# Performance work log

Hardware: AMD Instinct MI355X
Metric: run time of the kernel (lower is better)

Reference implementation:

```python
import jax, jax.numpy as jnp
import numpy as np

B, N, C = 8, 4096, 768
H, M = 12, 64          # num_heads, num_landmarks
D = C // H             # head_dim = 64


def setup_inputs() -> dict:
    key = jax.random.key(0)
    k1, k2, k3, k4 = jax.random.split(key, 4)
    s = 0.02
    return {
        "x": jax.random.normal(k1, (B, N, C), dtype=jnp.float32),
        "w_qkv": jax.random.normal(k2, (3 * C, C), dtype=jnp.float32) * s,
        "w_proj": jax.random.normal(k3, (C, C), dtype=jnp.float32) * s,
        "b_proj": jax.random.normal(k4, (C,), dtype=jnp.float32) * s,
    }


def iterative_inv(mat, n_iter=6):
    # mat: [B, H, M, M]; Newton-Schulz cubic iteration for pseudo-inverse
    I = jnp.eye(mat.shape[-1], dtype=mat.dtype)
    K = mat
    # init: K^T / max_j(sum_i K_ij)  per (B,H)
    scale = jnp.max(jnp.sum(K, axis=-2), axis=-1)[:, :, None, None]
    V = jnp.swapaxes(K, -1, -2) / scale
    for _ in range(n_iter):
        KV = K @ V
        V = 0.25 * V @ (13.0 * I - KV @ (15.0 * I - KV @ (7.0 * I - KV)))
    return V


def reference(x, w_qkv, w_proj, b_proj):
    b, n, c = x.shape
    qkv = (x @ w_qkv.T).reshape(b, n, 3, H, D).transpose(2, 0, 3, 1, 4)  # [3,B,H,N,D]
    Q, K, V = qkv[0], qkv[1], qkv[2]
    Q = Q / (D ** 0.5)
    # landmark pooling (N % M == 0 path): segment means of length N//M
    Kl = K.reshape(b, H, M, n // M, D).mean(axis=-2)  # [B,H,M,D]
    Ql = Q.reshape(b, H, M, n // M, D).mean(axis=-2)  # [B,H,M,D]
    kernel1 = jax.nn.softmax(jnp.einsum('bhnd,bhmd->bhnm', Q, Kl), axis=-1)   # [B,H,N,M]
    kernel2 = jax.nn.softmax(jnp.einsum('bhmd,bhld->bhml', Ql, Kl), axis=-1)  # [B,H,M,M]
    kernel3 = jax.nn.softmax(jnp.einsum('bhmd,bhnd->bhmn', Ql, K), axis=-1)   # [B,H,M,N]
    SV = (kernel1 @ iterative_inv(kernel2)) @ (kernel3 @ V)  # [B,H,N,D]
    SV = SV.transpose(0, 2, 1, 3).reshape(b, n, c)
    out = SV @ w_proj.T + b_proj
    out = out + V.transpose(0, 2, 1, 3).reshape(b, n, c)
    return out
```

## Files before the change

### kernel.cpp

```cpp
#include <hip/hip_runtime.h>
#include <hip/hip_bf16.h>
#include <stdint.h>

typedef __bf16 bf16;
typedef __bf16 bf16x8 __attribute__((ext_vector_type(8)));
typedef __bf16 bf16x4 __attribute__((ext_vector_type(4)));
typedef float f32x4 __attribute__((ext_vector_type(4)));

#define B_ 8
#define N_ 4096
#define C_ 768
#define H_ 12
#define M_ 64
#define D_ 64
#define NT_ 32768
#define C3_ 2304

typedef __attribute__((address_space(3))) void lds_void_t;
typedef const __attribute__((address_space(1))) void gvoid_t;

__device__ __forceinline__ void gl_lds16(const void* gsrc, void* ldst) {
  __builtin_amdgcn_global_load_lds((gvoid_t*)(uintptr_t)gsrc,
                                   (lds_void_t*)(uintptr_t)ldst, 16, 0, 0);
}

__device__ __forceinline__ f32x4 mfma16(bf16x8 a, bf16x8 b, f32x4 c) {
  return __builtin_amdgcn_mfma_f32_16x16x32_bf16(a, b, c, 0, 0, 0);
}

#define VMW8 asm volatile("s_waitcnt vmcnt(8)" ::: "memory")
#define VMW4 asm volatile("s_waitcnt vmcnt(4)" ::: "memory")
#define VMW0 asm volatile("s_waitcnt vmcnt(0)" ::: "memory")
#define LGKM0 asm volatile("s_waitcnt lgkmcnt(0)" ::: "memory")
#define RAWBAR() { __builtin_amdgcn_s_barrier(); __builtin_amdgcn_sched_barrier(0); }

__global__ void k_cvt(const float* __restrict__ in, bf16* __restrict__ out, int n4) {
  const int stride = gridDim.x * blockDim.x;
  for (int i = blockIdx.x * blockDim.x + threadIdx.x; i < n4; i += stride) {
    f32x4 v = *(const f32x4*)(in + (size_t)i * 4);
    bf16x4 o;
    o[0] = (bf16)v[0]; o[1] = (bf16)v[1]; o[2] = (bf16)v[2]; o[3] = (bf16)v[3];
    *(bf16x4*)(out + (size_t)i * 4) = o;
  }
}

__global__ __launch_bounds__(512, 2) void k_qkv(
    const bf16* __restrict__ xbf, const bf16* __restrict__ wbf,
    bf16* __restrict__ Qb, bf16* __restrict__ Kb, bf16* __restrict__ Vb,
    float* __restrict__ Qlf, float* __restrict__ Klf)
{
  __shared__ bf16 As[4][8192];
  __shared__ bf16 Bs[4][8192];
  const int t = threadIdx.x;
  const int wave = t >> 6, lane = t & 63;
  const int l15 = lane & 15, l16 = lane >> 4;

  const int bid = blockIdx.x;
  const int swz = (bid & 7) * 144 + (bid >> 3);
  const int bt = swz / 9, ct = swz % 9;
  const int row0 = bt * 256, col0 = ct * 256;
  const int wr = wave >> 2, wc = wave & 3;

  const int srow = t >> 2;
  const int scol = (((t & 3) ^ ((t >> 3) & 3)) << 3);
  const bf16* gaBase = xbf + (size_t)(row0 + srow) * C_ + scol;
  const bf16* gbBase = wbf + (size_t)(col0 + srow) * C_ + scol;

  const int aoff = (wr * 128 + l15) * 32 + ((l16 ^ ((l15 >> 1) & 3)) << 3);
  const int boff = (wc * 64 + l15) * 32 + ((l16 ^ ((l15 >> 1) & 3)) << 3);

  f32x4 acc[8][4] = {};

#define QSTAGE(kt3) {                                                            \
    const int sb_ = (kt3) & 3;                                                   \
    gl_lds16(gaBase + (size_t)0 * C_ + (kt3) * 32, &As[sb_][t * 8]);             \
    gl_lds16(gbBase + (size_t)0 * C_ + (kt3) * 32, &Bs[sb_][t * 8]);             \
    gl_lds16(gaBase + (size_t)128 * C_ + (kt3) * 32, &As[sb_][(t + 512) * 8]);   \
    gl_lds16(gbBase + (size_t)128 * C_ + (kt3) * 32, &Bs[sb_][(t + 512) * 8]); }

#define QKSTEP(kt, DO_STAGE, VMW_) {                                             \
    const bf16* as_ = As[(kt) & 3];                                              \
    const bf16* bs_ = Bs[(kt) & 3];                                              \
    if (DO_STAGE) QSTAGE((kt) + 3);                                              \
    bf16x8 bfr[4], afr[8];                                                       \
    _Pragma("unroll")                                                            \
    for (int j = 0; j < 4; ++j) bfr[j] = *(const bf16x8*)&bs_[boff + j * 512];   \
    _Pragma("unroll")                                                            \
    for (int i = 0; i < 8; ++i) afr[i] = *(const bf16x8*)&as_[aoff + i * 512];   \
    __builtin_amdgcn_s_setprio(1);                                               \
    _Pragma("unroll")                                                            \
    for (int i = 0; i < 8; ++i)                                                  \
      _Pragma("unroll")                                                          \
      for (int j = 0; j < 4; ++j)                                                \
        acc[i][j] = mfma16(afr[i], bfr[j], acc[i][j]);                           \
    __builtin_amdgcn_s_setprio(0);                                               \
    VMW_;                                                                        \
    LGKM0;                                                                       \
    RAWBAR(); }

  QSTAGE(0); QSTAGE(1); QSTAGE(2);
  VMW8;
  RAWBAR();

#pragma unroll 4
  for (int kt = 0; kt < 20; ++kt) { QKSTEP(kt, true, VMW8); }
  QKSTEP(20, true, VMW8);
  QKSTEP(21, false, VMW4);
  QKSTEP(22, false, VMW0);
  {
    const bf16* as_ = As[23 & 3];
    const bf16* bs_ = Bs[23 & 3];
    bf16x8 bfr[4], afr[8];
#pragma unroll
    for (int j = 0; j < 4; ++j) bfr[j] = *(const bf16x8*)&bs_[boff + j * 512];
#pragma unroll
    for (int i = 0; i < 8; ++i) afr[i] = *(const bf16x8*)&as_[aoff + i * 512];
#pragma unroll
    for (int i = 0; i < 8; ++i)
#pragma unroll
      for (int j = 0; j < 4; ++j)
        acc[i][j] = mfma16(afr[i], bfr[j], acc[i][j]);
  }
#undef QKSTEP
#undef QSTAGE

  const int colblock = col0 + wc * 64;
  const int which = colblock / C_;
  const int h = (colblock % C_) / D_;
  const int b = row0 >> 12;
  const int n_base = (row0 & (N_ - 1)) + wr * 128;
  bf16* dst = (which == 0) ? Qb : (which == 1) ? Kb : Vb;
  const float scale = (which == 0) ? 0.125f : 1.0f;
  const size_t base = ((size_t)(b * H_ + h) * N_ + n_base) * D_;
#pragma unroll
  for (int i = 0; i < 8; ++i)
#pragma unroll
    for (int q = 0; q < 4; ++q) {
      const int rloc = i * 16 + l16 * 4 + q;
#pragma unroll
      for (int j = 0; j < 4; ++j) {
        const int d = j * 16 + l15;
        dst[base + (size_t)rloc * D_ + d] = (bf16)(acc[i][j][q] * scale);
      }
    }
  if (which < 2) {
    float* lmout = (which == 0) ? Qlf : Klf;
#pragma unroll
    for (int g = 0; g < 2; ++g) {
      const int m = (n_base >> 6) + g;
#pragma unroll
      for (int j = 0; j < 4; ++j) {
        float s = 0.f;
#pragma unroll
        for (int i = 4 * g; i < 4 * g + 4; ++i)
#pragma unroll
          for (int q = 0; q < 4; ++q) s += acc[i][j][q];
        s *= scale;
        s += __shfl_xor(s, 16);
        s += __shfl_xor(s, 32);
        if (l16 == 0)
          lmout[((size_t)(b * H_ + h) * M_ + m) * D_ + j * 16 + lane] = s * (1.0f / 64.0f);
      }
    }
  }
}

__global__ __launch_bounds__(512, 1) void k_inv(
    const float* __restrict__ Qlf, const float* __restrict__ Klf,
    float* __restrict__ pinv, bf16* __restrict__ Qlb, bf16* __restrict__ Klb)
{
  __shared__ float K2[4096];
  __shared__ float Vm[4096];
  __shared__ float KV[4096];
  __shared__ float T1[4096];
  __shared__ float U1[4096];
  __shared__ float tmp64[64];
  __shared__ float sscale;
  const int t = threadIdx.x;
  const int bh = blockIdx.x;
  const size_t off = (size_t)bh * 4096;
  for (int idx = t; idx < 4096; idx += 512) {
    const float q = Qlf[off + idx];
    T1[idx] = q;
    Qlb[off + idx] = (bf16)q;
  }
  for (int idx = t; idx < 4096; idx += 512) {
    const int r = idx >> 6, c = idx & 63;
    const float k = Klf[off + idx];
    U1[c * 64 + r] = k;
    Klb[off + idx] = (bf16)k;
  }
  __syncthreads();
  const int j0 = (t & 15) * 4;
  const int i0 = (t >> 4) * 2;

  auto MMstep = [&](const float* A, const float* Bm, float* O, float dg, float sg, float al) {
    float r2[2][4] = {};
    for (int k = 0; k < 64; ++k) {
      f32x4 bv = *(const f32x4*)&Bm[k * 64 + j0];
      const float a0 = A[(i0 + 0) * 64 + k];
      const float a1 = A[(i0 + 1) * 64 + k];
#pragma unroll
      for (int jj = 0; jj < 4; ++jj) { r2[0][jj] += a0 * bv[jj]; r2[1][jj] += a1 * bv[jj]; }
    }
#pragma unroll
    for (int ii = 0; ii < 2; ++ii)
#pragma unroll
      for (int jj = 0; jj < 4; ++jj)
        O[(i0 + ii) * 64 + j0 + jj] = al * (dg * A[(i0 + ii) * 64 + (j0 + jj)] + sg * r2[ii][jj]);
    __syncthreads();
  };

  {
    float r2[2][4] = {};
    for (int k = 0; k < 64; ++k) {
      f32x4 bv = *(const f32x4*)&U1[k * 64 + j0];
      const float a0 = T1[(i0 + 0) * 64 + k];
      const float a1 = T1[(i0 + 1) * 64 + k];
#pragma unroll
      for (int jj = 0; jj < 4; ++jj) { r2[0][jj] += a0 * bv[jj]; r2[1][jj] += a1 * bv[jj]; }
    }
#pragma unroll
    for (int ii = 0; ii < 2; ++ii)
#pragma unroll
      for (int jj = 0; jj < 4; ++jj)
        K2[(i0 + ii) * 64 + j0 + jj] = __expf(r2[ii][jj]);
  }
  __syncthreads();
  if (t < 64) {
    float s = 0.f;
    for (int k = 0; k < 64; ++k) s += K2[t * 64 + k];
    tmp64[t] = 1.0f / s;
  }
  __syncthreads();
  for (int idx = t; idx < 4096; idx += 512) K2[idx] *= tmp64[idx >> 6];
  __syncthreads();
  if (t < 64) {
    float s = 0.f;
    for (int i = 0; i < 64; ++i) s += K2[i * 64 + t];
    tmp64[t] = s;
  }
  __syncthreads();
  if (t == 0) {
    float mx = tmp64[0];
    for (int j2 = 1; j2 < 64; ++j2) mx = fmaxf(mx, tmp64[j2]);
    sscale = 1.0f / mx;
  }
  __syncthreads();
  for (int idx = t; idx < 4096; idx += 512) {
    const int r = idx >> 6, c = idx & 63;
    Vm[idx] = K2[c * 64 + r] * sscale;
  }
  __syncthreads();

  float* pV = Vm;
  float* pT = T1;
  for (int it = 0; it < 6; ++it) {
    MMstep(K2, pV, KV, 0.f, 1.f, 1.f);
    MMstep(KV, KV, pT, 7.f, -1.f, 1.f);
    MMstep(KV, pT, U1, 15.f, -1.f, 1.f);
    MMstep(pV, U1, pT, 13.f, -1.f, 0.25f);
    float* sw = pV; pV = pT; pT = sw;
  }
  for (int idx = t; idx < 4096; idx += 512) pinv[off + idx] = pV[idx];
}

__global__ __launch_bounds__(256, 2) void k_k3v(
    const bf16* __restrict__ Qlb, const bf16* __restrict__ Kb, const bf16* __restrict__ Vb,
    float* __restrict__ Zacc, float* __restrict__ rowsum_g)
{
  __shared__ bf16 Qls[64 * 64];
  __shared__ bf16 Ks[128 * 64];
  __shared__ bf16 Vs[128 * 64];
  __shared__ bf16 Ps[64 * 128];
  __shared__ float rs[64];
  const int t = threadIdx.x, wave = t >> 6, lane = t & 63;
  const int bh = blockIdx.x >> 3;
  const int chunk = blockIdx.x & 7;
  const size_t kvbase = (size_t)bh * N_ * D_ + (size_t)chunk * 512 * D_;
  {
    const bf16* g = Qlb + (size_t)bh * 4096;
    gl_lds16(g + t * 8, &Qls[t * 8]);
    gl_lds16(g + (t + 256) * 8, &Qls[(t + 256) * 8]);
  }
  if (t < 64) rs[t] = 0.f;
  f32x4 z[4] = {};
  for (int st = 0; st < 4; ++st) {
    const bf16* gk = Kb + kvbase + (size_t)st * 128 * D_;
    const bf16* gv = Vb + kvbase + (size_t)st * 128 * D_;
#pragma unroll
    for (int c = 0; c < 4; ++c) {
      gl_lds16(gk + (t + c * 256) * 8, &Ks[(t + c * 256) * 8]);
      gl_lds16(gv + (t + c * 256) * 8, &Vs[(t + c * 256) * 8]);
    }
    __syncthreads();
    f32x4 sacc[4][2] = {};
#pragma unroll
    for (int kk = 0; kk < 2; ++kk) {
      bf16x8 af[4], bk[2];
#pragma unroll
      for (int i = 0; i < 4; ++i)
        af[i] = *(const bf16x8*)&Qls[(i * 16 + (lane & 15)) * 64 + kk * 32 + 8 * (lane >> 4)];
#pragma unroll
      for (int j2 = 0; j2 < 2; ++j2)
        bk[j2] = *(const bf16x8*)&Ks[(wave * 32 + j2 * 16 + (lane & 15)) * 64 + kk * 32 + 8 * (lane >> 4)];
#pragma unroll
      for (int i = 0; i < 4; ++i)
#pragma unroll
        for (int j2 = 0; j2 < 2; ++j2)
          sacc[i][j2] = mfma16(af[i], bk[j2], sacc[i][j2]);
    }
#pragma unroll
    for (int i = 0; i < 4; ++i)
#pragma unroll
      for (int q = 0; q < 4; ++q) {
        const float e0 = __expf(sacc[i][0][q]);
        const float e1 = __expf(sacc[i][1][q]);
        const int m = i * 16 + (lane >> 4) * 4 + q;
        Ps[m * 128 + wave * 32 + (lane & 15)] = (bf16)e0;
        Ps[m * 128 + wave * 32 + 16 + (lane & 15)] = (bf16)e1;
        float p = e0 + e1;
        p += __shfl_xor(p, 1); p += __shfl_xor(p, 2);
        p += __shfl_xor(p, 4); p += __shfl_xor(p, 8);
        if ((lane & 15) == 0) atomicAdd(&rs[m], p);
      }
    __syncthreads();
#pragma unroll
    for (int kk = 0; kk < 4; ++kk) {
      const int kbase = kk * 32 + 8 * (lane >> 4);
      const int d = wave * 16 + (lane & 15);
      bf16x8 bv;
#pragma unroll
      for (int e = 0; e < 8; ++e) bv[e] = Vs[(kbase + e) * 64 + d];
#pragma unroll
      for (int i = 0; i < 4; ++i) {
        bf16x8 ap = *(const bf16x8*)&Ps[(i * 16 + (lane & 15)) * 128 + kbase];
        z[i] = mfma16(ap, bv, z[i]);
      }
    }
    __syncthreads();
  }
  const size_t zbase = (size_t)bh * 4096;
#pragma unroll
  for (int i = 0; i < 4; ++i)
#pragma unroll
    for (int q = 0; q < 4; ++q) {
      const int m = i * 16 + (lane >> 4) * 4 + q;
      const int d = wave * 16 + (lane & 15);
      atomicAdd(&Zacc[zbase + m * 64 + d], z[i][q]);
    }
  if (t < 64) atomicAdd(&rowsum_g[bh * 64 + t], rs[t]);
}

__global__ __launch_bounds__(256, 1) void k_comb(
    const float* __restrict__ pinv, const float* __restrict__ Zacc,
    const float* __restrict__ rowsum_g, bf16* __restrict__ Wtb)
{
  __shared__ float Pv[4096];
  __shared__ float Zn[4096];
  const int t = threadIdx.x, bh = blockIdx.x;
  const size_t off = (size_t)bh * 4096;
  for (int idx = t; idx < 4096; idx += 256) Pv[idx] = pinv[off + idx];
  for (int idx = t; idx < 4096; idx += 256)
    Zn[idx] = Zacc[off + idx] / rowsum_g[bh * 64 + (idx >> 6)];
  __syncthreads();
  const int j0 = (t & 15) * 4, i0 = (t >> 4) * 4;
  float r[4][4] = {{0.f}};
  for (int k = 0; k < 64; ++k) {
    f32x4 bv = *(const f32x4*)&Zn[k * 64 + j0];
    float a[4];
#pragma unroll
    for (int ii = 0; ii < 4; ++ii) a[ii] = Pv[(i0 + ii) * 64 + k];
#pragma unroll
    for (int ii = 0; ii < 4; ++ii)
#pragma unroll
      for (int jj = 0; jj < 4; ++jj) r[ii][jj] += a[ii] * bv[jj];
  }
#pragma unroll
  for (int ii = 0; ii < 4; ++ii)
#pragma unroll
    for (int jj = 0; jj < 4; ++jj)
      Wtb[off + (size_t)(j0 + jj) * 64 + (i0 + ii)] = (bf16)r[ii][jj];
}

__global__ __launch_bounds__(256, 2) void k_sv(
    const bf16* __restrict__ Qb, const bf16* __restrict__ Klb,
    const bf16* __restrict__ Wtb, bf16* __restrict__ SVb)
{
  __shared__ bf16 Qs[128 * 64];
  __shared__ bf16 Kls[64 * 64];
  __shared__ bf16 Wts[64 * 64];
  __shared__ bf16 Ps[128 * 64];
  const int t = threadIdx.x, wave = t >> 6, lane = t & 63;
  const int bh = blockIdx.x >> 5;
  const int nt = blockIdx.x & 31;
  const int b = bh / H_, h = bh % H_;
  {
    const bf16* gq = Qb + (size_t)bh * N_ * D_ + (size_t)nt * 128 * D_;
#pragma unroll
    for (int c = 0; c < 4; ++c) gl_lds16(gq + (t + c * 256) * 8, &Qs[(t + c * 256) * 8]);
    const bf16* gkl = Klb + (size_t)bh * 4096;
    gl_lds16(gkl + t * 8, &Kls[t * 8]);
    gl_lds16(gkl + (t + 256) * 8, &Kls[(t + 256) * 8]);
    const bf16* gw = Wtb + (size_t)bh * 4096;
    gl_lds16(gw + t * 8, &Wts[t * 8]);
    gl_lds16(gw + (t + 256) * 8, &Wts[(t + 256) * 8]);
  }
  __syncthreads();
  f32x4 sacc[2][4] = {};
#pragma unroll
  for (int kk = 0; kk < 2; ++kk) {
    bf16x8 af[2], bl[4];
#pragma unroll
    for (int r = 0; r < 2; ++r)
      af[r] = *(const bf16x8*)&Qs[(wave * 32 + r * 16 + (lane & 15)) * 64 + kk * 32 + 8 * (lane >> 4)];
#pragma unroll
    for (int j = 0; j < 4; ++j)
      bl[j] = *(const bf16x8*)&Kls[(j * 16 + (lane & 15)) * 64 + kk * 32 + 8 * (lane >> 4)];
#pragma unroll
    for (int r = 0; r < 2; ++r)
#pragma unroll
      for (int j = 0; j < 4; ++j)
        sacc[r][j] = mfma16(af[r], bl[j], sacc[r][j]);
  }
#pragma unroll
  for (int r = 0; r < 2; ++r)
#pragma unroll
    for (int q = 0; q < 4; ++q) {
      float e[4]; float s = 0.f;
#pragma unroll
      for (int j = 0; j < 4; ++j) { e[j] = __expf(sacc[r][j][q]); s += e[j]; }
      s += __shfl_xor(s, 1); s += __shfl_xor(s, 2);
      s += __shfl_xor(s, 4); s += __shfl_xor(s, 8);
      const float is = 1.0f / s;
      const int row = wave * 32 + r * 16 + (lane >> 4) * 4 + q;
#pragma unroll
      for (int j = 0; j < 4; ++j)
        Ps[row * 64 + j * 16 + (lane & 15)] = (bf16)(e[j] * is);
    }
  __syncthreads();
  f32x4 oacc[2][4] = {};
#pragma unroll
  for (int kk = 0; kk < 2; ++kk) {
    bf16x8 af[2], bw[4];
#pragma unroll
    for (int r = 0; r < 2; ++r)
      af[r] = *(const bf16x8*)&Ps[(wave * 32 + r * 16 + (lane & 15)) * 64 + kk * 32 + 8 * (lane >> 4)];
#pragma unroll
    for (int j = 0; j < 4; ++j)
      bw[j] = *(const bf16x8*)&Wts[(j * 16 + (lane & 15)) * 64 + kk * 32 + 8 * (lane >> 4)];
#pragma unroll
    for (int r = 0; r < 2; ++r)
#pragma unroll
      for (int j = 0; j < 4; ++j)
        oacc[r][j] = mfma16(af[r], bw[j], oacc[r][j]);
  }
  const size_t outbase = ((size_t)b * N_ + (size_t)nt * 128) * C_ + h * 64;
#pragma unroll
  for (int r = 0; r < 2; ++r)
#pragma unroll
    for (int q = 0; q < 4; ++q) {
      const int row = wave * 32 + r * 16 + (lane >> 4) * 4 + q;
#pragma unroll
      for (int j = 0; j < 4; ++j)
        SVb[outbase + (size_t)row * C_ + j * 16 + (lane & 15)] = (bf16)(oacc[r][j][q]);
    }
}

__global__ __launch_bounds__(256, 2) void k_proj(
    const bf16* __restrict__ SVb, const bf16* __restrict__ wpb,
    const float* __restrict__ bproj, const bf16* __restrict__ Vb,
    float* __restrict__ outp)
{
  __shared__ bf16 As[4][4096];
  __shared__ bf16 Bs[4][4096];
  const int t = threadIdx.x;
  const int wave = t >> 6, lane = t & 63;
  const int l15 = lane & 15, l16 = lane >> 4;
  const int bid = blockIdx.x;
  const int swz = (bid & 7) * 192 + (bid >> 3);
  const int bt = swz / 6, ct = swz % 6;
  const int row0 = bt * 128, col0 = ct * 128;
  const int wr = wave >> 1, wc = wave & 1;

  const int srow = t >> 2;
  const int scol = (((t & 3) ^ ((t >> 3) & 3)) << 3);
  const bf16* ga = SVb + (size_t)(row0 + srow) * C_ + scol;
  const bf16* gb = wpb + (size_t)(col0 + srow) * C_ + scol;

  const int aoff = (wr * 64 + l15) * 32 + ((l16 ^ ((l15 >> 1) & 3)) << 3);
  const int boff = (wc * 64 + l15) * 32 + ((l16 ^ ((l15 >> 1) & 3)) << 3);

  f32x4 acc[4][4] = {};

#define PSTAGE(kt3) {                                                          \
    const int sb_ = (kt3) & 3;                                                 \
    gl_lds16(ga + (size_t)0 * C_ + (kt3) * 32, &As[sb_][t * 8]);               \
    gl_lds16(gb + (size_t)0 * C_ + (kt3) * 32, &Bs[sb_][t * 8]);               \
    gl_lds16(ga + (size_t)64 * C_ + (kt3) * 32, &As[sb_][(t + 256) * 8]);      \
    gl_lds16(gb + (size_t)64 * C_ + (kt3) * 32, &Bs[sb_][(t + 256) * 8]); }

#define PKSTEP(kt, DO_STAGE, VMW_) {                                           \
    const bf16* as_ = As[(kt) & 3];                                            \
    const bf16* bs_ = Bs[(kt) & 3];                                            \
    if (DO_STAGE) PSTAGE((kt) + 3);                                            \
    bf16x8 afr[4], bfr[4];                                                     \
    _Pragma("unroll")                                                          \
    for (int j = 0; j < 4; ++j) bfr[j] = *(const bf16x8*)&bs_[boff + j * 512]; \
    _Pragma("unroll")                                                          \
    for (int i = 0; i < 4; ++i) afr[i] = *(const bf16x8*)&as_[aoff + i * 512]; \
    __builtin_amdgcn_s_setprio(1);                                             \
    _Pragma("unroll")                                                          \
    for (int i = 0; i < 4; ++i)                                                \
      _Pragma("unroll")                                                        \
      for (int j = 0; j < 4; ++j)                                              \
        acc[i][j] = mfma16(afr[i], bfr[j], acc[i][j]);                         \
    __builtin_amdgcn_s_setprio(0);                                             \
    VMW_;                                                                      \
    LGKM0;                                                                     \
    RAWBAR(); }

  PSTAGE(0); PSTAGE(1); PSTAGE(2);
  VMW8;
  RAWBAR();

#pragma unroll 4
  for (int kt = 0; kt < 20; ++kt) { PKSTEP(kt, true, VMW8); }
  PKSTEP(20, true, VMW8);
  PKSTEP(21, false, VMW4);
  PKSTEP(22, false, VMW0);
  {
    const bf16* as_ = As[3];
    const bf16* bs_ = Bs[3];
    bf16x8 afr[4], bfr[4];
#pragma unroll
    for (int j = 0; j < 4; ++j) bfr[j] = *(const bf16x8*)&bs_[boff + j * 512];
#pragma unroll
    for (int i = 0; i < 4; ++i) afr[i] = *(const bf16x8*)&as_[aoff + i * 512];
#pragma unroll
    for (int i = 0; i < 4; ++i)
#pragma unroll
      for (int j = 0; j < 4; ++j)
        acc[i][j] = mfma16(afr[i], bfr[j], acc[i][j]);
  }
#undef PKSTEP
#undef PSTAGE

#pragma unroll
  for (int i = 0; i < 4; ++i)
#pragma unroll
    for (int q = 0; q < 4; ++q) {
      const int row = row0 + wr * 64 + i * 16 + l16 * 4 + q;
      const int b = row >> 12, n = row & (N_ - 1);
#pragma unroll
      for (int j = 0; j < 4; ++j) {
        const int col = col0 + wc * 64 + j * 16 + l15;
        const int h = col >> 6, d = col & 63;
        const float v = acc[i][j][q] + bproj[col] +
                        (float)Vb[((size_t)(b * H_ + h) * N_ + n) * D_ + d];
        outp[(size_t)row * C_ + col] = v;
      }
    }
}

extern "C" void kernel_launch(void* const* d_in, const int* in_sizes, int n_in,
                              void* d_out, int out_size, void* d_ws, size_t ws_size,
                              hipStream_t stream) {
  const float* x = (const float*)d_in[0];
  const float* wqkv = (const float*)d_in[1];
  const float* wproj = (const float*)d_in[2];
  const float* bproj = (const float*)d_in[3];
  float* outp = (float*)d_out;
  char* ws = (char*)d_ws;

  size_t off = 0;
  auto take = [&](size_t bytes) { char* p = ws + off; off += bytes; return p; };
  bf16* xbf     = (bf16*)take(50331648);
  bf16* wqkvbf  = (bf16*)take(3538944);
  bf16* wprojbf = (bf16*)take(1179648);
  bf16* Qb      = (bf16*)take(50331648);
  bf16* Kb      = (bf16*)take(50331648);
  bf16* Vb      = (bf16*)take(50331648);
  float* Qlf    = (float*)take(1572864);
  float* Klf    = (float*)take(1572864);
  bf16* Qlb     = (bf16*)take(786432);
  bf16* Klb     = (bf16*)take(786432);
  float* pinvp  = (float*)take(1572864);
  float* Zacc   = (float*)take(1572864);
  float* rowsum = (float*)take(24576);
  bf16* Wtb     = (bf16*)take(786432);
  bf16* SVb     = xbf;

  hipMemsetAsync(Zacc, 0, 1572864 + 24576, stream);

  k_cvt<<<2048, 256, 0, stream>>>(x, xbf, 25165824 / 4);
  k_cvt<<<432, 256, 0, stream>>>(wqkv, wqkvbf, 1769472 / 4);
  k_cvt<<<144, 256, 0, stream>>>(wproj, wprojbf, 589824 / 4);
  k_qkv<<<1152, 512, 0, stream>>>(xbf, wqkvbf, Qb, Kb, Vb, Qlf, Klf);
  k_inv<<<96, 512, 0, stream>>>(Qlf, Klf, pinvp, Qlb, Klb);
  k_k3v<<<768, 256, 0, stream>>>(Qlb, Kb, Vb, Zacc, rowsum);
  k_comb<<<96, 256, 0, stream>>>(pinvp, Zacc, rowsum, Wtb);
  k_sv<<<96 * 32, 256, 0, stream>>>(Qb, Klb, Wtb, SVb);
  k_proj<<<1536, 256, 0, stream>>>(SVb, wprojbf, bproj, Vb, outp);
}
```

Baseline: 392.0 us.

## Load QKV weight fragments directly to registers, drop B tile from LDS

```diff
diff --git a/kernel.cpp b/kernel.cpp
--- a/kernel.cpp
+++ b/kernel.cpp
@@ -49,8 +49,7 @@
     bf16* __restrict__ Qb, bf16* __restrict__ Kb, bf16* __restrict__ Vb,
     float* __restrict__ Qlf, float* __restrict__ Klf)
 {
-  __shared__ bf16 As[4][8192];
-  __shared__ bf16 Bs[4][8192];
+  __shared__ bf16 As[3][8192];
   const int t = threadIdx.x;
   const int wave = t >> 6, lane = t & 63;
   const int l15 = lane & 15, l16 = lane >> 4;
@@ -64,65 +63,57 @@
   const int srow = t >> 2;
   const int scol = (((t & 3) ^ ((t >> 3) & 3)) << 3);
   const bf16* gaBase = xbf + (size_t)(row0 + srow) * C_ + scol;
-  const bf16* gbBase = wbf + (size_t)(col0 + srow) * C_ + scol;
 
   const int aoff = (wr * 128 + l15) * 32 + ((l16 ^ ((l15 >> 1) & 3)) << 3);
-  const int boff = (wc * 64 + l15) * 32 + ((l16 ^ ((l15 >> 1) & 3)) << 3);
+
+  const bf16* bp0 = wbf + (size_t)(col0 + wc * 64 + 0 * 16 + l15) * C_ + 8 * l16;
+  const bf16* bp1 = wbf + (size_t)(col0 + wc * 64 + 1 * 16 + l15) * C_ + 8 * l16;
+  const bf16* bp2 = wbf + (size_t)(col0 + wc * 64 + 2 * 16 + l15) * C_ + 8 * l16;
+  const bf16* bp3 = wbf + (size_t)(col0 + wc * 64 + 3 * 16 + l15) * C_ + 8 * l16;
 
   f32x4 acc[8][4] = {};
-
-#define QSTAGE(kt3) {                                                            \
-    const int sb_ = (kt3) & 3;                                                   \
-    gl_lds16(gaBase + (size_t)0 * C_ + (kt3) * 32, &As[sb_][t * 8]);             \
-    gl_lds16(gbBase + (size_t)0 * C_ + (kt3) * 32, &Bs[sb_][t * 8]);             \
-    gl_lds16(gaBase + (size_t)128 * C_ + (kt3) * 32, &As[sb_][(t + 512) * 8]);   \
-    gl_lds16(gbBase + (size_t)128 * C_ + (kt3) * 32, &Bs[sb_][(t + 512) * 8]); }
-
-#define QKSTEP(kt, DO_STAGE, VMW_) {                                             \
-    const bf16* as_ = As[(kt) & 3];                                              \
-    const bf16* bs_ = Bs[(kt) & 3];                                              \
-    if (DO_STAGE) QSTAGE((kt) + 3);                                              \
-    bf16x8 bfr[4], afr[8];                                                       \
-    _Pragma("unroll")                                                            \
-    for (int j = 0; j < 4; ++j) bfr[j] = *(const bf16x8*)&bs_[boff + j * 512];   \
-    _Pragma("unroll")                                                            \
-    for (int i = 0; i < 8; ++i) afr[i] = *(const bf16x8*)&as_[aoff + i * 512];   \
-    __builtin_amdgcn_s_setprio(1);                                               \
-    _Pragma("unroll")                                                            \
-    for (int i = 0; i < 8; ++i)                                                  \
-      _Pragma("unroll")                                                          \
-      for (int j = 0; j < 4; ++j)                                                \
-        acc[i][j] = mfma16(afr[i], bfr[j], acc[i][j]);                           \
-    __builtin_amdgcn_s_setprio(0);                                               \
-    VMW_;                                                                        \
-    LGKM0;                                                                       \
-    RAWBAR(); }
-
-  QSTAGE(0); QSTAGE(1); QSTAGE(2);
-  VMW8;
+  bf16x8 breg[2][4];
+
+#define ASTAGE(kt2) {                                                           \
+    gl_lds16(gaBase + (kt2) * 32, &As[(kt2) % 3][t * 8]);                       \
+    gl_lds16(gaBase + (size_t)128 * C_ + (kt2) * 32, &As[(kt2) % 3][(t + 512) * 8]); }
+
+#define BLOAD(kt1) {                                                            \
+    breg[(kt1) & 1][0] = *(const bf16x8*)(bp0 + (kt1) * 32);                    \
+    breg[(kt1) & 1][1] = *(const bf16x8*)(bp1 + (kt1) * 32);                    \
+    breg[(kt1) & 1][2] = *(const bf16x8*)(bp2 + (kt1) * 32);                    \
+    breg[(kt1) & 1][3] = *(const bf16x8*)(bp3 + (kt1) * 32); }
+
+#define QSTEP(kt, DO_STAGE, DO_BLOAD, DO_SYNC) {                                \
+    if (DO_STAGE) ASTAGE((kt) + 2);                                             \
+    if (DO_BLOAD) BLOAD((kt) + 1);                                              \
+    const bf16* as_ = As[(kt) % 3];                                             \
+    bf16x8 afr[8];                                                              \
+    _Pragma("unroll")                                                           \
+    for (int i = 0; i < 8; ++i) afr[i] = *(const bf16x8*)&as_[aoff + i * 512];  \
+    __builtin_amdgcn_s_setprio(1);                                              \
+    _Pragma("unroll")                                                           \
+    for (int i = 0; i < 8; ++i)                                                 \
+      _Pragma("unroll")                                                         \
+      for (int j = 0; j < 4; ++j)                                               \
+        acc[i][j] = mfma16(afr[i], breg[(kt) & 1][j], acc[i][j]);               \
+    __builtin_amdgcn_s_setprio(0);                                              \
+    if (DO_SYNC) { VMW0; LGKM0; RAWBAR(); } }
+
+  ASTAGE(0); ASTAGE(1); BLOAD(0);
+  VMW0;
   RAWBAR();
 
-#pragma unroll 4
-  for (int kt = 0; kt < 20; ++kt) { QKSTEP(kt, true, VMW8); }
-  QKSTEP(20, true, VMW8);
-  QKSTEP(21, false, VMW4);
-  QKSTEP(22, false, VMW0);
-  {
-    const bf16* as_ = As[23 & 3];
-    const bf16* bs_ = Bs[23 & 3];
-    bf16x8 bfr[4], afr[8];
-#pragma unroll
-    for (int j = 0; j < 4; ++j) bfr[j] = *(const bf16x8*)&bs_[boff + j * 512];
-#pragma unroll
-    for (int i = 0; i < 8; ++i) afr[i] = *(const bf16x8*)&as_[aoff + i * 512];
-#pragma unroll
-    for (int i = 0; i < 8; ++i)
-#pragma unroll
-      for (int j = 0; j < 4; ++j)
-        acc[i][j] = mfma16(afr[i], bfr[j], acc[i][j]);
-  }
-#undef QKSTEP
-#undef QSTAGE
+  QSTEP(0, 1, 1, 1)  QSTEP(1, 1, 1, 1)  QSTEP(2, 1, 1, 1)  QSTEP(3, 1, 1, 1)
+  QSTEP(4, 1, 1, 1)  QSTEP(5, 1, 1, 1)  QSTEP(6, 1, 1, 1)  QSTEP(7, 1, 1, 1)
+  QSTEP(8, 1, 1, 1)  QSTEP(9, 1, 1, 1)  QSTEP(10, 1, 1, 1) QSTEP(11, 1, 1, 1)
+  QSTEP(12, 1, 1, 1) QSTEP(13, 1, 1, 1) QSTEP(14, 1, 1, 1) QSTEP(15, 1, 1, 1)
+  QSTEP(16, 1, 1, 1) QSTEP(17, 1, 1, 1) QSTEP(18, 1, 1, 1) QSTEP(19, 1, 1, 1)
+  QSTEP(20, 1, 1, 1) QSTEP(21, 1, 1, 1) QSTEP(22, 0, 1, 1) QSTEP(23, 0, 0, 0)
+
+#undef QSTEP
+#undef BLOAD
+#undef ASTAGE
 
   const int colblock = col0 + wc * 64;
   const int which = colblock / C_;
```

Measured after the change: 453.8 us. 1.16x slower.
